# Performance work log

Hardware: AMD Instinct MI355X
Metric: run time of the kernel (lower is better)

## Reference

```python
import jax, jax.numpy as jnp
import numpy as np

B, L = 4, 2048
D_MODEL, D_STATE, D_CONV, N_BLOCKS = 128, 16, 8, 6
EXPAND = 2
D_INNER = EXPAND * D_MODEL          # 256
DT_RANK = (D_MODEL + 15) // 16      # 8
CONV_K = 7                          # pre_conv kernel


def setup_inputs() -> dict:
    key = jax.random.key(0)
    ks = jax.random.split(key, 10)
    f = lambda k, s: jax.random.normal(k, s, jnp.float32)
    sc = 0.02
    A_init = jnp.broadcast_to(
        jnp.log(jnp.arange(1, D_STATE + 1, dtype=jnp.float32)),
        (N_BLOCKS, D_INNER, D_STATE)) + 0.0
    return {
        "x": f(ks[0], (B, L, 1)),
        "pre_conv_w": f(ks[1], (D_MODEL, 1, CONV_K)) * sc,
        "pre_conv_b": jnp.zeros((D_MODEL,), jnp.float32),
        "ln_w": jnp.ones((N_BLOCKS, D_MODEL), jnp.float32),
        "ln_b": jnp.zeros((N_BLOCKS, D_MODEL), jnp.float32),
        "W_in": f(ks[2], (N_BLOCKS, 2 * D_INNER, D_MODEL)) * sc,
        "conv_w": f(ks[3], (N_BLOCKS, D_INNER, 1, D_CONV)) * sc,  # depthwise OIH
        "conv_b": jnp.zeros((N_BLOCKS, D_INNER), jnp.float32),
        "W_x": f(ks[4], (N_BLOCKS, DT_RANK + 2 * D_STATE, D_INNER)) * sc,
        "W_dt": f(ks[5], (N_BLOCKS, D_INNER, DT_RANK)) * sc,
        "b_dt": jnp.full((N_BLOCKS, D_INNER), -4.6, jnp.float32),  # softplus ~ 0.01
        "A_log": A_init,
        "D_skip": jnp.ones((N_BLOCKS, D_INNER), jnp.float32),
        "W_out": f(ks[6], (N_BLOCKS, D_MODEL, D_INNER)) * sc,
        "out_w": f(ks[7], (1, D_MODEL)) * sc,
        "out_b": jnp.zeros((1,), jnp.float32),
    }


def _layernorm(x, w, b, eps=1e-5):
    m = jnp.mean(x, axis=-1, keepdims=True)
    v = jnp.mean(jnp.square(x - m), axis=-1, keepdims=True)
    return (x - m) * jax.lax.rsqrt(v + eps) * w + b


def _mamba(x, W_in, cw, cb, W_x, W_dt, b_dt, A_log, D_skip, W_out):
    # x: (B, L, D_MODEL)
    xz = jnp.einsum('bld,ed->ble', x, W_in)            # (B,L,2E)
    xi, z = jnp.split(xz, 2, axis=-1)
    # depthwise causal conv over time
    xc = jax.lax.conv_general_dilated(
        xi.transpose(0, 2, 1), cw, window_strides=(1,),
        padding=[(D_CONV - 1, 0)],
        dimension_numbers=('NCH', 'OIH', 'NCH'),
        feature_group_count=D_INNER) + cb[None, :, None]
    xc = jax.nn.silu(xc).transpose(0, 2, 1)            # (B,L,E)
    dbl = jnp.einsum('ble,re->blr', xc, W_x)
    dt = dbl[..., :DT_RANK]
    Bm = dbl[..., DT_RANK:DT_RANK + D_STATE]           # (B,L,N)
    Cm = dbl[..., DT_RANK + D_STATE:]                  # (B,L,N)
    delta = jax.nn.softplus(jnp.einsum('blr,er->ble', dt, W_dt) + b_dt)
    A = -jnp.exp(A_log)                                # (E,N)

    def step(h, inp):
        d, b, c, u = inp                               # (B,E),(B,N),(B,N),(B,E)
        h = h * jnp.exp(d[..., None] * A) + (d * u)[..., None] * b[:, None, :]
        return h, jnp.einsum('ben,bn->be', h, c)

    h0 = jnp.zeros((x.shape[0], D_INNER, D_STATE), x.dtype)
    xs = (delta.transpose(1, 0, 2), Bm.transpose(1, 0, 2),
          Cm.transpose(1, 0, 2), xc.transpose(1, 0, 2))
    _, ys = jax.lax.scan(step, h0, xs)                 # ys: (L,B,E)
    y = ys.transpose(1, 0, 2) + D_skip * xc
    y = y * jax.nn.silu(z)
    return jnp.einsum('ble,de->bld', y, W_out)


def reference(x, pre_conv_w, pre_conv_b, ln_w, ln_b, W_in, conv_w, conv_b,
              W_x, W_dt, b_dt, A_log, D_skip, W_out, out_w, out_b):
    # pre_conv (1 -> d_model), SAME padding, then exact GELU
    h = jax.lax.conv_general_dilated(
        x.transpose(0, 2, 1), pre_conv_w, window_strides=(1,),
        padding=[(CONV_K // 2, CONV_K // 2)],
        dimension_numbers=('NCH', 'OIH', 'NCH')) + pre_conv_b[None, :, None]
    h = jax.nn.gelu(h, approximate=False).transpose(0, 2, 1)  # (B,L,D)

    def block(carry, p):
        lw, lb, Wi, cw, cb, Wx, Wdt, bdt, Alog, Dsk, Wo = p
        y = _mamba(_layernorm(carry, lw, lb), Wi, cw, cb, Wx, Wdt, bdt, Alog, Dsk, Wo)
        return carry + y, None                         # dropout is identity (eval)

    h, _ = jax.lax.scan(block, h, (ln_w, ln_b, W_in, conv_w, conv_b,
                                   W_x, W_dt, b_dt, A_log, D_skip, W_out))
    return (jnp.einsum('bld,od->blo', h, out_w) + out_b)[..., 0]  # (B,L)
```

## Files before the change

### kernel.cpp

```cpp
#include <hip/hip_runtime.h>
#include <hip/hip_bf16.h>
#include <hip/hip_cooperative_groups.h>
#include <math.h>

namespace cg = cooperative_groups;

#define BB 4
#define LL 2048
#define DM 128
#define DI 256
#define DS 16
#define DTR 8
#define NB 6
#define KPRE 7
#define KC 8
#define NC 64
#define CT 32
#define BL (BB*LL)
#define SU 4

typedef __attribute__((ext_vector_type(8))) short short8v;
typedef __attribute__((ext_vector_type(4))) float f32x4;


__device__ __forceinline__ void dev_preconv(int idx,
    const float* __restrict__ x, const float* __restrict__ w, const float* __restrict__ bias,
    float* __restrict__ h, const float* __restrict__ Wi, const float* __restrict__ Wo,
    __hip_bfloat16* __restrict__ wi, __hip_bfloat16* __restrict__ wo) {
    int d = idx & (DM - 1);
    int l = (idx >> 7) & (LL - 1);
    int b = idx >> 18;
    float acc = bias[d];
#pragma unroll
    for (int k = 0; k < KPRE; ++k) {
        int pos = l + k - 3;
        float xv = (pos >= 0 && pos < LL) ? x[b * LL + pos] : 0.f;
        acc = fmaf(xv, w[d * KPRE + k], acc);
    }
    h[idx] = 0.5f * acc * (1.f + erff(acc * 0.70710678118654752f));
    if (idx < NB * 2 * DI * DM) wi[idx] = __float2bfloat16(Wi[idx]);
    if (idx < NB * DM * DI)     wo[idx] = __float2bfloat16(Wo[idx]);
}

__device__ __forceinline__ void dev_ln_gemm1(int v, int wave, int lane,
    const float* __restrict__ h, const float* __restrict__ lw, const float* __restrict__ lb,
    const __hip_bfloat16* __restrict__ W, float* __restrict__ xz,
    __hip_bfloat16* As) {
    int tileM = v >> 2, tileN = v & 3;
    int mBase = tileM * 64, nBase = tileN * 128;
    for (int it = 0; it < 16; ++it) {
        int row = wave * 16 + it;
        int t = mBase + row;
        float v0 = h[t * DM + lane];
        float v1 = h[t * DM + lane + 64];
        float s = v0 + v1;
#pragma unroll
        for (int off = 32; off; off >>= 1) s += __shfl_xor(s, off);
        float mean = s * (1.f / 128.f);
        float d0 = v0 - mean, d1 = v1 - mean;
        float q = d0 * d0 + d1 * d1;
#pragma unroll
        for (int off = 32; off; off >>= 1) q += __shfl_xor(q, off);
        float rstd = rsqrtf(q * (1.f / 128.f) + 1e-5f);
        int sw = (row & 7) << 3;
        As[row * 128 + (lane ^ sw)]        = __float2bfloat16(d0 * rstd * lw[lane] + lb[lane]);
        As[row * 128 + ((lane + 64) ^ sw)] = __float2bfloat16(d1 * rstd * lw[lane + 64] + lb[lane + 64]);
    }
    __syncthreads();
    int r  = lane & 15;
    int kh = lane >> 4;
    f32x4 acc[4][2] = {};
    for (int k0 = 0; k0 < DM; k0 += 32) {
        short8v af[4], bf[2];
#pragma unroll
        for (int i = 0; i < 4; ++i) {
            int row = i * 16 + r;
            int cbk = (k0 >> 3) + kh;
            af[i] = *(const short8v*)&As[row * 128 + ((cbk ^ (row & 7)) << 3)];
        }
#pragma unroll
        for (int j = 0; j < 2; ++j)
            bf[j] = *(const short8v*)&W[(size_t)(nBase + wave * 32 + j * 16 + r) * DM + k0 + kh * 8];
#pragma unroll
        for (int i = 0; i < 4; ++i)
#pragma unroll
            for (int j = 0; j < 2; ++j)
                acc[i][j] = __builtin_amdgcn_mfma_f32_16x16x32_bf16(af[i], bf[j], acc[i][j], 0, 0, 0);
    }
#pragma unroll
    for (int i = 0; i < 4; ++i)
#pragma unroll
        for (int j = 0; j < 2; ++j)
#pragma unroll
            for (int rg = 0; rg < 4; ++rg) {
                size_t off = (size_t)(mBase + i * 16 + kh * 4 + rg) * (2 * DI)
                           + nBase + wave * 32 + j * 16 + r;
                xz[off] = acc[i][j][rg];
            }
    __syncthreads();
}

__device__ __forceinline__ void dev_conv_wx(int t, int lane,
    const float* __restrict__ xz, const float* __restrict__ cw, const float* __restrict__ cbs,
    const float* __restrict__ Wx, const float* __restrict__ Wdt, const float* __restrict__ bdt,
    float* __restrict__ xc, float* __restrict__ BC, float* __restrict__ delta) {
    int tl = t & (LL - 1);
    int b = t >> 11;
    float xv[4];
#pragma unroll
    for (int j = 0; j < 4; ++j) {
        int e = lane + 64 * j;
        float4 cw0 = *(const float4*)&cw[e * KC];
        float4 cw1 = *(const float4*)&cw[e * KC + 4];
        float wts[8] = {cw0.x, cw0.y, cw0.z, cw0.w, cw1.x, cw1.y, cw1.z, cw1.w};
        float acc = cbs[e];
#pragma unroll
        for (int k = 0; k < KC; ++k) {
            int pos = tl + k - (KC - 1);
            float v = (pos >= 0) ? xz[((size_t)(b * LL + pos) << 9) + e] : 0.f;
            acc = fmaf(v, wts[k], acc);
        }
        xv[j] = acc / (1.f + __expf(-acc));
        xc[((size_t)t << 8) + e] = xv[j];
    }
    float dt[8];
    float bcv = 0.f;
#pragma unroll
    for (int o = 0; o < 40; ++o) {
        const float* w = &Wx[o * DI];
        float s = xv[0] * w[lane];
        s = fmaf(xv[1], w[lane + 64], s);
        s = fmaf(xv[2], w[lane + 128], s);
        s = fmaf(xv[3], w[lane + 192], s);
#pragma unroll
        for (int off = 32; off; off >>= 1) s += __shfl_xor(s, off);
        if (o < 8) dt[o] = s;
        else if (lane == o - 8) bcv = s;
    }
    if (lane < 32) BC[((size_t)t << 5) + lane] = bcv;
#pragma unroll
    for (int j = 0; j < 4; ++j) {
        int e = lane + 64 * j;
        float s = bdt[e];
#pragma unroll
        for (int r = 0; r < 8; ++r) s = fmaf(dt[r], Wdt[e * 8 + r], s);
        delta[((size_t)t << 8) + e] = fmaxf(s, 0.f) + log1pf(__expf(-fabsf(s)));
    }
}

__device__ __forceinline__ void dev_scan1(int blk, int tid,
    const float* __restrict__ delta, const float* __restrict__ xc, const float* __restrict__ BC,
    const float* __restrict__ A_log, float* __restrict__ P, float* __restrict__ hend) {
    int eg = blk & 3;
    int c = (blk >> 2) & (NC - 1);
    int b = blk >> 8;
    int e = eg * 64 + (tid >> 2);
    int ng = tid & 3;
    float4 al = *(const float4*)&A_log[e * DS + 4 * ng];
    float Aen[4] = {-__expf(al.x), -__expf(al.y), -__expf(al.z), -__expf(al.w)};
    float h[4] = {}, Pl[4] = {1.f, 1.f, 1.f, 1.f};
    int base = b * LL + c * CT;
    const float* dp = delta + (size_t)base * DI + e;
    const float* up = xc + (size_t)base * DI + e;
    const float* bp = BC + (size_t)base * 32 + 4 * ng;
    for (int l0 = 0; l0 < CT; l0 += SU) {
        float d[SU], u[SU];
        float4 bm[SU];
#pragma unroll
        for (int j = 0; j < SU; ++j) {
            d[j]  = dp[(l0 + j) * DI];
            u[j]  = up[(l0 + j) * DI];
            bm[j] = *(const float4*)&bp[(l0 + j) * 32];
        }
#pragma unroll
        for (int j = 0; j < SU; ++j) {
            float du = d[j] * u[j];
            float a0 = __expf(d[j] * Aen[0]);
            float a1 = __expf(d[j] * Aen[1]);
            float a2 = __expf(d[j] * Aen[2]);
            float a3 = __expf(d[j] * Aen[3]);
            h[0] = fmaf(h[0], a0, du * bm[j].x);
            h[1] = fmaf(h[1], a1, du * bm[j].y);
            h[2] = fmaf(h[2], a2, du * bm[j].z);
            h[3] = fmaf(h[3], a3, du * bm[j].w);
            Pl[0] *= a0; Pl[1] *= a1; Pl[2] *= a2; Pl[3] *= a3;
        }
    }
    size_t oidx = (((size_t)(b * NC + c)) * DI + e) * DS + 4 * ng;
    *(float4*)&P[oidx]    = make_float4(Pl[0], Pl[1], Pl[2], Pl[3]);
    *(float4*)&hend[oidx] = make_float4(h[0], h[1], h[2], h[3]);
}

__device__ __forceinline__ void dev_carry(int gtid,
    const float* __restrict__ P, const float* __restrict__ hend, float* __restrict__ hin) {
    int n = gtid & 15;
    int e = (gtid >> 4) & 255;
    int b = gtid >> 12;
    float carry = 0.f;
    for (int c = 0; c < NC; ++c) {
        size_t idx = (((size_t)(b * NC + c)) * DI + e) * DS + n;
        hin[idx] = carry;
        carry = fmaf(P[idx], carry, hend[idx]);
    }
}

__device__ __forceinline__ void dev_scan3(int blk, int tid,
    const float* __restrict__ delta, const float* __restrict__ xc, const float* __restrict__ BC,
    const float* __restrict__ A_log, const float* __restrict__ hin, const float* __restrict__ xz,
    const float* __restrict__ Dsk, __hip_bfloat16* __restrict__ y) {
    int eg = blk & 3;
    int c = (blk >> 2) & (NC - 1);
    int b = blk >> 8;
    int e = eg * 64 + (tid >> 2);
    int ng = tid & 3;
    float4 al = *(const float4*)&A_log[e * DS + 4 * ng];
    float Aen[4] = {-__expf(al.x), -__expf(al.y), -__expf(al.z), -__expf(al.w)};
    float dsk = Dsk[e];
    size_t hidx = (((size_t)(b * NC + c)) * DI + e) * DS + 4 * ng;
    float4 h4 = *(const float4*)&hin[hidx];
    float h[4] = {h4.x, h4.y, h4.z, h4.w};
    int base = b * LL + c * CT;
    const float* dp = delta + (size_t)base * DI + e;
    const float* up = xc + (size_t)base * DI + e;
    const float* bp = BC + (size_t)base * 32 + 4 * ng;
    const float* zp = xz + ((size_t)base << 9) + DI + e;
    __hip_bfloat16* yp = y + (size_t)base * DI + e;
    for (int l0 = 0; l0 < CT; l0 += SU) {
        float d[SU], u[SU], zv[SU];
        float4 bm[SU], cm[SU];
#pragma unroll
        for (int j = 0; j < SU; ++j) {
            d[j]  = dp[(l0 + j) * DI];
            u[j]  = up[(l0 + j) * DI];
            bm[j] = *(const float4*)&bp[(l0 + j) * 32];
            cm[j] = *(const float4*)&bp[(l0 + j) * 32 + 16];
            zv[j] = zp[(size_t)(l0 + j) << 9];
        }
#pragma unroll
        for (int j = 0; j < SU; ++j) {
            float du = d[j] * u[j];
            float a0 = __expf(d[j] * Aen[0]);
            float a1 = __expf(d[j] * Aen[1]);
            float a2 = __expf(d[j] * Aen[2]);
            float a3 = __expf(d[j] * Aen[3]);
            h[0] = fmaf(h[0], a0, du * bm[j].x);
            h[1] = fmaf(h[1], a1, du * bm[j].y);
            h[2] = fmaf(h[2], a2, du * bm[j].z);
            h[3] = fmaf(h[3], a3, du * bm[j].w);
            float yc = h[0] * cm[j].x;
            yc = fmaf(h[1], cm[j].y, yc);
            yc = fmaf(h[2], cm[j].z, yc);
            yc = fmaf(h[3], cm[j].w, yc);
            yc += __shfl_xor(yc, 1);
            yc += __shfl_xor(yc, 2);
            if (ng == 0) {
                float z = zv[j];
                float val = (yc + dsk * u[j]) * (z / (1.f + __expf(-z)));
                yp[(l0 + j) * DI] = __float2bfloat16(val);
            }
        }
    }
}

__device__ __forceinline__ void dev_gemm2(int v, int wave, int lane,
    const __hip_bfloat16* __restrict__ A, const __hip_bfloat16* __restrict__ W,
    float* __restrict__ C) {
    int mBase = v * 16;
    int r  = lane & 15;
    int kh = lane >> 4;
    f32x4 acc[2] = {};
    for (int k0 = 0; k0 < DI; k0 += 32) {
        short8v af = *(const short8v*)&A[(size_t)(mBase + r) * DI + k0 + kh * 8];
        short8v bf[2];
#pragma unroll
        for (int j = 0; j < 2; ++j)
            bf[j] = *(const short8v*)&W[(size_t)(wave * 32 + j * 16 + r) * DI + k0 + kh * 8];
#pragma unroll
        for (int j = 0; j < 2; ++j)
            acc[j] = __builtin_amdgcn_mfma_f32_16x16x32_bf16(af, bf[j], acc[j], 0, 0, 0);
    }
#pragma unroll
    for (int j = 0; j < 2; ++j)
#pragma unroll
        for (int rg = 0; rg < 4; ++rg) {
            size_t off = (size_t)(mBase + kh * 4 + rg) * DM + wave * 32 + j * 16 + r;
            C[off] += acc[j][rg];
        }
}

__device__ __forceinline__ void dev_out(int t, int lane,
    const float* __restrict__ h, const float* __restrict__ ow, const float* __restrict__ ob,
    float* __restrict__ out) {
    float s = h[t * DM + lane] * ow[lane] + h[t * DM + lane + 64] * ow[lane + 64];
#pragma unroll
    for (int off = 32; off; off >>= 1) s += __shfl_xor(s, off);
    if (lane == 0) out[t] = s + ob[0];
}


struct MegaArgs {
    const float *x, *pcw, *pcb, *ln_w, *ln_b, *W_in, *conv_w, *conv_b;
    const float *W_x, *W_dt, *b_dt, *A_log, *D_skip, *W_out, *out_w, *out_b;
    float *h, *xz, *xc, *BC, *delta, *P, *hend, *hin, *out;
    __hip_bfloat16 *y_bf, *wi_bf, *wo_bf;
};

__global__ __launch_bounds__(256) void k_mega(MegaArgs a) {
    __shared__ __hip_bfloat16 As[64 * 128];
    cg::grid_group g = cg::this_grid();
    int bid = blockIdx.x, tid = threadIdx.x;
    int nb = gridDim.x;
    int wave = tid >> 6, lane = tid & 63;

    for (int v = bid; v < (BB * LL * DM) / 256; v += nb)
        dev_preconv(v * 256 + tid, a.x, a.pcw, a.pcb, a.h, a.W_in, a.W_out, a.wi_bf, a.wo_bf);
    g.sync();

    for (int blk = 0; blk < NB; ++blk) {
        for (int v = bid; v < 512; v += nb)
            dev_ln_gemm1(v, wave, lane, a.h, a.ln_w + blk * DM, a.ln_b + blk * DM,
                         a.wi_bf + (size_t)blk * 2 * DI * DM, a.xz, As);
        g.sync();
        for (int v = bid; v < BL / 4; v += nb)
            dev_conv_wx(v * 4 + wave, lane, a.xz, a.conv_w + (size_t)blk * DI * KC,
                        a.conv_b + blk * DI, a.W_x + (size_t)blk * 40 * DI,
                        a.W_dt + (size_t)blk * DI * DTR, a.b_dt + blk * DI,
                        a.xc, a.BC, a.delta);
        g.sync();
        for (int v = bid; v < BB * NC * 4; v += nb)
            dev_scan1(v, tid, a.delta, a.xc, a.BC, a.A_log + (size_t)blk * DI * DS, a.P, a.hend);
        g.sync();
        for (int v = bid; v < (BB * DI * DS) / 256; v += nb)
            dev_carry(v * 256 + tid, a.P, a.hend, a.hin);
        g.sync();
        for (int v = bid; v < BB * NC * 4; v += nb)
            dev_scan3(v, tid, a.delta, a.xc, a.BC, a.A_log + (size_t)blk * DI * DS,
                      a.hin, a.xz, a.D_skip + blk * DI, a.y_bf);
        g.sync();
        for (int v = bid; v < 512; v += nb)
            dev_gemm2(v, wave, lane, a.y_bf, a.wo_bf + (size_t)blk * DM * DI, a.h);
        g.sync();
    }

    for (int v = bid; v < BL / 4; v += nb)
        dev_out(v * 4 + wave, lane, a.h, a.out_w, a.out_b, a.out);
}


__global__ void w_preconv(const float* x, const float* w, const float* bias, float* h,
                          const float* Wi, const float* Wo,
                          __hip_bfloat16* wi, __hip_bfloat16* wo) {
    dev_preconv(blockIdx.x * 256 + threadIdx.x, x, w, bias, h, Wi, Wo, wi, wo);
}
__global__ __launch_bounds__(256) void w_ln_gemm1(const float* h, const float* lw, const float* lb,
                                                  const __hip_bfloat16* W, float* xz) {
    __shared__ __hip_bfloat16 As[64 * 128];
    dev_ln_gemm1(blockIdx.x, threadIdx.x >> 6, threadIdx.x & 63, h, lw, lb, W, xz, As);
}
__global__ __launch_bounds__(256) void w_conv_wx(const float* xz, const float* cw, const float* cbs,
                                                 const float* Wx, const float* Wdt, const float* bdt,
                                                 float* xc, float* BC, float* delta) {
    dev_conv_wx(blockIdx.x * 4 + (threadIdx.x >> 6), threadIdx.x & 63,
                xz, cw, cbs, Wx, Wdt, bdt, xc, BC, delta);
}
__global__ __launch_bounds__(256) void w_scan1(const float* delta, const float* xc, const float* BC,
                                               const float* A_log, float* P, float* hend) {
    dev_scan1(blockIdx.x, threadIdx.x, delta, xc, BC, A_log, P, hend);
}
__global__ void w_carry(const float* P, const float* hend, float* hin) {
    dev_carry(blockIdx.x * 256 + threadIdx.x, P, hend, hin);
}
__global__ __launch_bounds__(256) void w_scan3(const float* delta, const float* xc, const float* BC,
                                               const float* A_log, const float* hin, const float* xz,
                                               const float* Dsk, __hip_bfloat16* y) {
    dev_scan3(blockIdx.x, threadIdx.x, delta, xc, BC, A_log, hin, xz, Dsk, y);
}
__global__ __launch_bounds__(256) void w_gemm2(const __hip_bfloat16* A, const __hip_bfloat16* W,
                                               float* C) {
    dev_gemm2(blockIdx.x, threadIdx.x >> 6, threadIdx.x & 63, A, W, C);
}
__global__ void w_out(const float* h, const float* ow, const float* ob, float* out) {
    dev_out(blockIdx.x * 4 + (threadIdx.x >> 6), threadIdx.x & 63, h, ow, ob, out);
}

extern "C" void kernel_launch(void* const* d_in, const int* in_sizes, int n_in,
                              void* d_out, int out_size, void* d_ws, size_t ws_size,
                              hipStream_t stream) {
    (void)in_sizes; (void)n_in; (void)out_size; (void)ws_size;
    const float* x      = (const float*)d_in[0];
    const float* pcw    = (const float*)d_in[1];
    const float* pcb    = (const float*)d_in[2];
    const float* ln_w   = (const float*)d_in[3];
    const float* ln_b   = (const float*)d_in[4];
    const float* W_in   = (const float*)d_in[5];
    const float* conv_w = (const float*)d_in[6];
    const float* conv_b = (const float*)d_in[7];
    const float* W_x    = (const float*)d_in[8];
    const float* W_dt   = (const float*)d_in[9];
    const float* b_dt   = (const float*)d_in[10];
    const float* A_log  = (const float*)d_in[11];
    const float* D_skip = (const float*)d_in[12];
    const float* W_out  = (const float*)d_in[13];
    const float* out_w  = (const float*)d_in[14];
    const float* out_b  = (const float*)d_in[15];

    float* ws    = (float*)d_ws;
    float* h     = ws;
    float* xz    = h     + (size_t)BL * DM;
    float* xc    = xz    + (size_t)BL * 2 * DI;
    float* BC    = xc    + (size_t)BL * DI;
    float* delta = BC    + (size_t)BL * 2 * DS;
    float* P     = delta + (size_t)BL * DI;
    float* hend  = P     + (size_t)BB * NC * DI * DS;
    float* hin   = hend  + (size_t)BB * NC * DI * DS;
    __hip_bfloat16* y_bf  = (__hip_bfloat16*)(hin + (size_t)BB * NC * DI * DS);
    __hip_bfloat16* wi_bf = y_bf  + (size_t)BL * DI;
    __hip_bfloat16* wo_bf = wi_bf + (size_t)NB * 2 * DI * DM;

    int dev = 0;
    (void)hipGetDevice(&dev);
    int coopAttr = 0;
    (void)hipDeviceGetAttribute(&coopAttr, hipDeviceAttributeCooperativeLaunch, dev);
    int numCU = 0;
    (void)hipDeviceGetAttribute(&numCU, hipDeviceAttributeMultiprocessorCount, dev);
    int maxBpCU = 0;
    (void)hipOccupancyMaxActiveBlocksPerMultiprocessor(&maxBpCU, k_mega, 256, 0);
    int grid = maxBpCU * numCU;
    if (grid > 512) grid = 512;

    bool launched = false;
    if (coopAttr && grid > 0) {
        MegaArgs ma = {x, pcw, pcb, ln_w, ln_b, W_in, conv_w, conv_b,
                       W_x, W_dt, b_dt, A_log, D_skip, W_out, out_w, out_b,
                       h, xz, xc, BC, delta, P, hend, hin, (float*)d_out,
                       y_bf, wi_bf, wo_bf};
        void* kp[] = {&ma};
        hipError_t e = hipLaunchCooperativeKernel((void*)k_mega, dim3(grid), dim3(256), kp, 0, stream);
        launched = (e == hipSuccess);
        if (!launched) (void)hipGetLastError();
    }

    if (!launched) {
        w_preconv<<<(BB * LL * DM) / 256, 256, 0, stream>>>(x, pcw, pcb, h, W_in, W_out, wi_bf, wo_bf);
        for (int blk = 0; blk < NB; ++blk) {
            w_ln_gemm1<<<512, 256, 0, stream>>>(
                h, ln_w + blk * DM, ln_b + blk * DM, wi_bf + (size_t)blk * 2 * DI * DM, xz);
            w_conv_wx<<<BL / 4, 256, 0, stream>>>(
                xz, conv_w + (size_t)blk * DI * KC, conv_b + blk * DI,
                W_x + (size_t)blk * 40 * DI, W_dt + (size_t)blk * DI * DTR,
                b_dt + blk * DI, xc, BC, delta);
            w_scan1<<<BB * NC * 4, 256, 0, stream>>>(
                delta, xc, BC, A_log + (size_t)blk * DI * DS, P, hend);
            w_carry<<<(BB * DI * DS) / 256, 256, 0, stream>>>(P, hend, hin);
            w_scan3<<<BB * NC * 4, 256, 0, stream>>>(
                delta, xc, BC, A_log + (size_t)blk * DI * DS, hin, xz, D_skip + blk * DI, y_bf);
            w_gemm2<<<BL / 16, 256, 0, stream>>>(y_bf, wo_bf + (size_t)blk * DM * DI, h);
        }
        w_out<<<BL / 4, 256, 0, stream>>>(h, out_w, out_b, (float*)d_out);
    }
}
```

Baseline: 565.3 us.

## Fuse conv/x-proj/scan phases per chunk in shared memory, cutting grid syncs

Each block now owns one 16-timestep chunk and runs conv, x-projection, delta and the chunk-local scan in one phase, keeping xc, delta and B/C in LDS. It then runs the second scan, gating and the output GEMM for the same chunk from that LDS state. This removes two grid-wide syncs per layer and the global round trips through the xc, delta, BC and y buffers. In exchange the chunk count doubles, so the serial carry pass is longer, and each block uses more LDS, which may lower occupancy. The cooperative path now runs only if exactly 512 blocks are co-resident, otherwise it falls back to separate kernels.

```diff
diff --git a/kernel.cpp b/kernel.cpp
--- a/kernel.cpp
+++ b/kernel.cpp
@@ -14,8 +14,9 @@
 #define NB 6
 #define KPRE 7
 #define KC 8
-#define NC 64
-#define CT 32
+#define NC 128
+#define CT 16
+#define NCHUNK (BB*NC)
 #define BL (BB*LL)
 #define SU 4
 
@@ -100,6 +101,192 @@
     __syncthreads();
 }
 
+__device__ __forceinline__ void dev_fusedA(int chunk, int tid,
+    const float* __restrict__ xz, const float* __restrict__ cw, const float* __restrict__ cbs,
+    const float* __restrict__ Wx, const float* __restrict__ Wdt, const float* __restrict__ bdt,
+    const float* __restrict__ A_log, float* __restrict__ P, float* __restrict__ hend,
+    float (*xc_s)[DI], float (*dl_s)[DI], float (*bc_s)[32]) {
+    int c = chunk & (NC - 1);
+    int b = chunk >> 7;
+    int wave = tid >> 6, lane = tid & 63;
+    float wts[4][8], cb4[4];
+#pragma unroll
+    for (int j = 0; j < 4; ++j) {
+        int e = lane + 64 * j;
+        float4 c0 = *(const float4*)&cw[e * KC];
+        float4 c1 = *(const float4*)&cw[e * KC + 4];
+        wts[j][0]=c0.x; wts[j][1]=c0.y; wts[j][2]=c0.z; wts[j][3]=c0.w;
+        wts[j][4]=c1.x; wts[j][5]=c1.y; wts[j][6]=c1.z; wts[j][7]=c1.w;
+        cb4[j] = cbs[e];
+    }
+    for (int i = 0; i < 4; ++i) {
+        int lt = wave * 4 + i;
+        int tl = c * CT + lt;
+        float xv[4];
+#pragma unroll
+        for (int j = 0; j < 4; ++j) {
+            int e = lane + 64 * j;
+            float acc = cb4[j];
+#pragma unroll
+            for (int k = 0; k < KC; ++k) {
+                int pos = tl + k - (KC - 1);
+                float v = (pos >= 0) ? xz[((size_t)(b * LL + pos) << 9) + e] : 0.f;
+                acc = fmaf(v, wts[j][k], acc);
+            }
+            xv[j] = acc / (1.f + __expf(-acc));
+            xc_s[lt][e] = xv[j];
+        }
+        float dt8[8];
+        float bcv = 0.f;
+#pragma unroll
+        for (int o = 0; o < 40; ++o) {
+            const float* w = &Wx[o * DI];
+            float s = xv[0] * w[lane];
+            s = fmaf(xv[1], w[lane + 64], s);
+            s = fmaf(xv[2], w[lane + 128], s);
+            s = fmaf(xv[3], w[lane + 192], s);
+#pragma unroll
+            for (int off = 32; off; off >>= 1) s += __shfl_xor(s, off);
+            if (o < 8) dt8[o] = s;
+            else if (lane == o - 8) bcv = s;
+        }
+        if (lane < 32) bc_s[lt][lane] = bcv;
+#pragma unroll
+        for (int j = 0; j < 4; ++j) {
+            int e = lane + 64 * j;
+            float s = bdt[e];
+#pragma unroll
+            for (int r = 0; r < 8; ++r) s = fmaf(dt8[r], Wdt[e * 8 + r], s);
+            dl_s[lt][e] = fmaxf(s, 0.f) + log1pf(__expf(-fabsf(s)));
+        }
+    }
+    __syncthreads();
+    int e = tid;
+    float d16[CT], u16[CT];
+#pragma unroll
+    for (int l = 0; l < CT; ++l) { d16[l] = dl_s[l][e]; u16[l] = xc_s[l][e]; }
+#pragma unroll
+    for (int ng = 0; ng < 4; ++ng) {
+        float4 al = *(const float4*)&A_log[e * DS + 4 * ng];
+        float Aen[4] = {-__expf(al.x), -__expf(al.y), -__expf(al.z), -__expf(al.w)};
+        float hh[4] = {}, Pl[4] = {1.f, 1.f, 1.f, 1.f};
+#pragma unroll
+        for (int l = 0; l < CT; ++l) {
+            float du = d16[l] * u16[l];
+            float4 bm = *(const float4*)&bc_s[l][4 * ng];
+            float a0 = __expf(d16[l] * Aen[0]);
+            float a1 = __expf(d16[l] * Aen[1]);
+            float a2 = __expf(d16[l] * Aen[2]);
+            float a3 = __expf(d16[l] * Aen[3]);
+            hh[0] = fmaf(hh[0], a0, du * bm.x);
+            hh[1] = fmaf(hh[1], a1, du * bm.y);
+            hh[2] = fmaf(hh[2], a2, du * bm.z);
+            hh[3] = fmaf(hh[3], a3, du * bm.w);
+            Pl[0] *= a0; Pl[1] *= a1; Pl[2] *= a2; Pl[3] *= a3;
+        }
+        size_t oidx = (((size_t)(b * NC + c)) * DI + e) * DS + 4 * ng;
+        *(float4*)&P[oidx]    = make_float4(Pl[0], Pl[1], Pl[2], Pl[3]);
+        *(float4*)&hend[oidx] = make_float4(hh[0], hh[1], hh[2], hh[3]);
+    }
+}
+
+__device__ __forceinline__ void dev_carry(int gtid,
+    const float* __restrict__ P, const float* __restrict__ hend, float* __restrict__ hin) {
+    int n = gtid & 15;
+    int e = (gtid >> 4) & 255;
+    int b = gtid >> 12;
+    float carry = 0.f;
+    for (int c = 0; c < NC; ++c) {
+        size_t idx = (((size_t)(b * NC + c)) * DI + e) * DS + n;
+        hin[idx] = carry;
+        carry = fmaf(P[idx], carry, hend[idx]);
+    }
+}
+
+__device__ __forceinline__ void dev_fusedB(int chunk, int tid,
+    const float* __restrict__ A_log, const float* __restrict__ hin,
+    const float* __restrict__ xz, const float* __restrict__ Dsk,
+    const __hip_bfloat16* __restrict__ Wo, float* __restrict__ hout,
+    const float (*xc_s)[DI], const float (*dl_s)[DI], const float (*bc_s)[32],
+    __hip_bfloat16 (*y_s)[DI + 8]) {
+    int c = chunk & (NC - 1);
+    int b = chunk >> 7;
+    int base = b * LL + c * CT;
+    int e = tid;
+    float d16[CT], u16[CT], yacc[CT];
+    float dsk = Dsk[e];
+#pragma unroll
+    for (int l = 0; l < CT; ++l) {
+        d16[l] = dl_s[l][e];
+        u16[l] = xc_s[l][e];
+        yacc[l] = dsk * u16[l];
+    }
+#pragma unroll
+    for (int ng = 0; ng < 4; ++ng) {
+        float4 al = *(const float4*)&A_log[e * DS + 4 * ng];
+        float Aen[4] = {-__expf(al.x), -__expf(al.y), -__expf(al.z), -__expf(al.w)};
+        float4 h4 = *(const float4*)&hin[(((size_t)(b * NC + c)) * DI + e) * DS + 4 * ng];
+        float hh[4] = {h4.x, h4.y, h4.z, h4.w};
+#pragma unroll
+        for (int l = 0; l < CT; ++l) {
+            float du = d16[l] * u16[l];
+            float4 bm = *(const float4*)&bc_s[l][4 * ng];
+            float4 cm = *(const float4*)&bc_s[l][16 + 4 * ng];
+            float a0 = __expf(d16[l] * Aen[0]);
+            float a1 = __expf(d16[l] * Aen[1]);
+            float a2 = __expf(d16[l] * Aen[2]);
+            float a3 = __expf(d16[l] * Aen[3]);
+            hh[0] = fmaf(hh[0], a0, du * bm.x);
+            hh[1] = fmaf(hh[1], a1, du * bm.y);
+            hh[2] = fmaf(hh[2], a2, du * bm.z);
+            hh[3] = fmaf(hh[3], a3, du * bm.w);
+            float p = hh[0] * cm.x;
+            p = fmaf(hh[1], cm.y, p);
+            p = fmaf(hh[2], cm.z, p);
+            p = fmaf(hh[3], cm.w, p);
+            yacc[l] += p;
+        }
+    }
+#pragma unroll
+    for (int l = 0; l < CT; ++l) {
+        float z = xz[((size_t)(base + l) << 9) + DI + e];
+        float val = yacc[l] * (z / (1.f + __expf(-z)));
+        y_s[l][e] = __float2bfloat16(val);
+    }
+    __syncthreads();
+    int wave = tid >> 6, lane = tid & 63;
+    int r  = lane & 15;
+    int kh = lane >> 4;
+    f32x4 acc[2] = {};
+    for (int k0 = 0; k0 < DI; k0 += 32) {
+        short8v af = *(const short8v*)&y_s[r][k0 + kh * 8];
+        short8v bf[2];
+#pragma unroll
+        for (int j = 0; j < 2; ++j)
+            bf[j] = *(const short8v*)&Wo[(size_t)(wave * 32 + j * 16 + r) * DI + k0 + kh * 8];
+#pragma unroll
+        for (int j = 0; j < 2; ++j)
+            acc[j] = __builtin_amdgcn_mfma_f32_16x16x32_bf16(af, bf[j], acc[j], 0, 0, 0);
+    }
+#pragma unroll
+    for (int j = 0; j < 2; ++j)
+#pragma unroll
+        for (int rg = 0; rg < 4; ++rg) {
+            size_t off = (size_t)(base + kh * 4 + rg) * DM + wave * 32 + j * 16 + r;
+            hout[off] += acc[j][rg];
+        }
+}
+
+__device__ __forceinline__ void dev_out(int t, int lane,
+    const float* __restrict__ h, const float* __restrict__ ow, const float* __restrict__ ob,
+    float* __restrict__ out) {
+    float s = h[t * DM + lane] * ow[lane] + h[t * DM + lane + 64] * ow[lane + 64];
+#pragma unroll
+    for (int off = 32; off; off >>= 1) s += __shfl_xor(s, off);
+    if (lane == 0) out[t] = s + ob[0];
+}
+
+
 __device__ __forceinline__ void dev_conv_wx(int t, int lane,
     const float* __restrict__ xz, const float* __restrict__ cw, const float* __restrict__ cbs,
     const float* __restrict__ Wx, const float* __restrict__ Wdt, const float* __restrict__ bdt,
@@ -153,7 +340,7 @@
     const float* __restrict__ A_log, float* __restrict__ P, float* __restrict__ hend) {
     int eg = blk & 3;
     int c = (blk >> 2) & (NC - 1);
-    int b = blk >> 8;
+    int b = blk >> 9;
     int e = eg * 64 + (tid >> 2);
     int ng = tid & 3;
     float4 al = *(const float4*)&A_log[e * DS + 4 * ng];
@@ -191,33 +378,19 @@
     *(float4*)&hend[oidx] = make_float4(h[0], h[1], h[2], h[3]);
 }
 
-__device__ __forceinline__ void dev_carry(int gtid,
-    const float* __restrict__ P, const float* __restrict__ hend, float* __restrict__ hin) {
-    int n = gtid & 15;
-    int e = (gtid >> 4) & 255;
-    int b = gtid >> 12;
-    float carry = 0.f;
-    for (int c = 0; c < NC; ++c) {
-        size_t idx = (((size_t)(b * NC + c)) * DI + e) * DS + n;
-        hin[idx] = carry;
-        carry = fmaf(P[idx], carry, hend[idx]);
-    }
-}
-
 __device__ __forceinline__ void dev_scan3(int blk, int tid,
     const float* __restrict__ delta, const float* __restrict__ xc, const float* __restrict__ BC,
     const float* __restrict__ A_log, const float* __restrict__ hin, const float* __restrict__ xz,
     const float* __restrict__ Dsk, __hip_bfloat16* __restrict__ y) {
     int eg = blk & 3;
     int c = (blk >> 2) & (NC - 1);
-    int b = blk >> 8;
+    int b = blk >> 9;
     int e = eg * 64 + (tid >> 2);
     int ng = tid & 3;
     float4 al = *(const float4*)&A_log[e * DS + 4 * ng];
     float Aen[4] = {-__expf(al.x), -__expf(al.y), -__expf(al.z), -__expf(al.w)};
     float dsk = Dsk[e];
-    size_t hidx = (((size_t)(b * NC + c)) * DI + e) * DS + 4 * ng;
-    float4 h4 = *(const float4*)&hin[hidx];
+    float4 h4 = *(const float4*)&hin[(((size_t)(b * NC + c)) * DI + e) * DS + 4 * ng];
     float h[4] = {h4.x, h4.y, h4.z, h4.w};
     int base = b * LL + c * CT;
     const float* dp = delta + (size_t)base * DI + e;
@@ -288,15 +461,6 @@
         }
 }
 
-__device__ __forceinline__ void dev_out(int t, int lane,
-    const float* __restrict__ h, const float* __restrict__ ow, const float* __restrict__ ob,
-    float* __restrict__ out) {
-    float s = h[t * DM + lane] * ow[lane] + h[t * DM + lane + 64] * ow[lane + 64];
-#pragma unroll
-    for (int off = 32; off; off >>= 1) s += __shfl_xor(s, off);
-    if (lane == 0) out[t] = s + ob[0];
-}
-
 
 struct MegaArgs {
     const float *x, *pcw, *pcb, *ln_w, *ln_b, *W_in, *conv_w, *conv_b;
@@ -307,6 +471,10 @@
 
 __global__ __launch_bounds__(256) void k_mega(MegaArgs a) {
     __shared__ __hip_bfloat16 As[64 * 128];
+    __shared__ float xc_s[CT][DI];
+    __shared__ float dl_s[CT][DI];
+    __shared__ float bc_s[CT][32];
+    __shared__ __hip_bfloat16 y_s[CT][DI + 8];
     cg::grid_group g = cg::this_grid();
     int bid = blockIdx.x, tid = threadIdx.x;
     int nb = gridDim.x;
@@ -321,24 +489,20 @@
             dev_ln_gemm1(v, wave, lane, a.h, a.ln_w + blk * DM, a.ln_b + blk * DM,
                          a.wi_bf + (size_t)blk * 2 * DI * DM, a.xz, As);
         g.sync();
-        for (int v = bid; v < BL / 4; v += nb)
-            dev_conv_wx(v * 4 + wave, lane, a.xz, a.conv_w + (size_t)blk * DI * KC,
-                        a.conv_b + blk * DI, a.W_x + (size_t)blk * 40 * DI,
-                        a.W_dt + (size_t)blk * DI * DTR, a.b_dt + blk * DI,
-                        a.xc, a.BC, a.delta);
-        g.sync();
-        for (int v = bid; v < BB * NC * 4; v += nb)
-            dev_scan1(v, tid, a.delta, a.xc, a.BC, a.A_log + (size_t)blk * DI * DS, a.P, a.hend);
+        if (bid < NCHUNK)
+            dev_fusedA(bid, tid, a.xz, a.conv_w + (size_t)blk * DI * KC,
+                       a.conv_b + blk * DI, a.W_x + (size_t)blk * 40 * DI,
+                       a.W_dt + (size_t)blk * DI * DTR, a.b_dt + blk * DI,
+                       a.A_log + (size_t)blk * DI * DS, a.P, a.hend,
+                       xc_s, dl_s, bc_s);
         g.sync();
         for (int v = bid; v < (BB * DI * DS) / 256; v += nb)
             dev_carry(v * 256 + tid, a.P, a.hend, a.hin);
         g.sync();
-        for (int v = bid; v < BB * NC * 4; v += nb)
-            dev_scan3(v, tid, a.delta, a.xc, a.BC, a.A_log + (size_t)blk * DI * DS,
-                      a.hin, a.xz, a.D_skip + blk * DI, a.y_bf);
-        g.sync();
-        for (int v = bid; v < 512; v += nb)
-            dev_gemm2(v, wave, lane, a.y_bf, a.wo_bf + (size_t)blk * DM * DI, a.h);
+        if (bid < NCHUNK)
+            dev_fusedB(bid, tid, a.A_log + (size_t)blk * DI * DS, a.hin, a.xz,
+                       a.D_skip + blk * DI, a.wo_bf + (size_t)blk * DM * DI, a.h,
+                       xc_s, dl_s, bc_s, y_s);
         g.sync();
     }
 
@@ -426,10 +590,10 @@
     int maxBpCU = 0;
     (void)hipOccupancyMaxActiveBlocksPerMultiprocessor(&maxBpCU, k_mega, 256, 0);
     int grid = maxBpCU * numCU;
-    if (grid > 512) grid = 512;
+    if (grid > NCHUNK) grid = NCHUNK;
 
     bool launched = false;
-    if (coopAttr && grid > 0) {
+    if (coopAttr && grid == NCHUNK) {
         MegaArgs ma = {x, pcw, pcb, ln_w, ln_b, W_in, conv_w, conv_b,
                        W_x, W_dt, b_dt, A_log, D_skip, W_out, out_w, out_b,
                        h, xz, xc, BC, delta, P, hend, hin, (float*)d_out,
```

After: 597.8 us. +5.8%, slower.
